# Kernel optimization log

Hardware: AMD Instinct MI355X
Metric: run time of the kernel (lower is better)

The kernel has to match this reference:

```python
import jax, jax.numpy as jnp
import numpy as np
from jax import lax

N_NODES = 100000
N_EDGES = 1600000
DIM = 64
N_GRAPHS = 128
OUT = 10
BN_EPS = 1e-5


def setup_inputs() -> dict:
    key = jax.random.key(0)
    ks = jax.random.split(key, 8)
    s = 1.0 / np.sqrt(DIM)
    x = jax.random.normal(ks[0], (N_NODES, DIM), dtype=jnp.float32)
    edge_index = jax.random.randint(ks[1], (2, N_EDGES), 0, N_NODES, dtype=jnp.int64)
    batch = jnp.sort(jax.random.randint(ks[2], (N_NODES,), 0, N_GRAPHS, dtype=jnp.int64))
    return {
        "x": x,
        "edge_index": edge_index,
        "batch": batch,
        "W1": jax.random.normal(ks[3], (5, DIM, DIM), dtype=jnp.float32) * s,
        "b1": jnp.zeros((5, DIM), jnp.float32),
        "gamma": jnp.ones((5, DIM), jnp.float32),
        "beta": jnp.zeros((5, DIM), jnp.float32),
        "rmean": jnp.zeros((5, DIM), jnp.float32),
        "rvar": jnp.ones((5, DIM), jnp.float32),
        "W2": jax.random.normal(ks[4], (5, DIM, DIM), dtype=jnp.float32) * s,
        "b2": jnp.zeros((5, DIM), jnp.float32),
        "lin1_w": jax.random.normal(ks[5], (DIM, DIM), dtype=jnp.float32) * s,
        "lin1_b": jnp.zeros((DIM,), jnp.float32),
        "lin2_w": jax.random.normal(ks[6], (DIM, OUT), dtype=jnp.float32) * s,
        "lin2_b": jnp.zeros((OUT,), jnp.float32),
    }


def reference(x, edge_index, batch, W1, b1, gamma, beta, rmean, rvar, W2, b2,
              lin1_w, lin1_b, lin2_w, lin2_b):
    n = x.shape[0]
    src, dst = edge_index[0], edge_index[1]

    def gin_layer(h, p):
        w1, bb1, g, bt, m, v, w2, bb2 = p
        # GINConv (eps=0): h_i <- MLP(h_i + sum_{j in N(i)} h_j)
        agg = jax.ops.segment_sum(h[src], dst, num_segments=n)
        h = h + agg
        h = h @ w1 + bb1
        h = (h - m) * lax.rsqrt(v + BN_EPS) * g + bt  # BatchNorm1d (eval)
        h = jax.nn.relu(h)
        h = jax.nn.relu(h @ w2 + bb2)
        return h, None

    h, _ = lax.scan(gin_layer, x, (W1, b1, gamma, beta, rmean, rvar, W2, b2))
    # global_add_pool over graphs in the batch
    pooled = jax.ops.segment_sum(h, batch, num_segments=N_GRAPHS)  # [G, dim]
    pooled = jax.nn.relu(pooled @ lin1_w + lin1_b)
    # dropout is identity in eval mode
    return pooled @ lin2_w + lin2_b  # [G, out]
```

## Files before the change

kernel.cpp:

```cpp
#include <hip/hip_runtime.h>

#define N_NODES  100000
#define N_EDGES  1600000
#define DIM      64
#define N_GRAPHS 128
#define OUT_DIM  10
#define SCAN_NB    196
#define SCAN_CHUNK 512
#define RANGE_BITS 14
#define RANGE_SIZE 16384
#define N_RANGES   7
#define NODE_PAD   (N_RANGES * RANGE_SIZE)
#define P_CHUNKS   512
#define P_EDGES    (N_EDGES / P_CHUNKS)
#define SUB        16

typedef unsigned int uint;
typedef unsigned short ushort;
typedef __attribute__((ext_vector_type(8))) short short8;
typedef __attribute__((ext_vector_type(4))) float f32x4;

__device__ __forceinline__ uint f2bf(float x) {
    uint b = __float_as_uint(x);
    b += 0x7fffu + ((b >> 16) & 1u);
    return b >> 16;
}


__global__ void count224_kernel(const int* __restrict__ dst, int* __restrict__ counts224) {
    __shared__ int cnt[8];
    const int c = blockIdx.x, tid = threadIdx.x;
    if (tid < 8) cnt[tid] = 0;
    __syncthreads();
    int c0 = 0, c1 = 0, c2 = 0, c3 = 0, c4 = 0, c5 = 0, c6 = 0;
    const int beg = c * P_EDGES, end = beg + P_EDGES;
    for (int i = beg + tid; i < end; i += 256) {
        int r = dst[i] >> RANGE_BITS;
        c0 += (r == 0); c1 += (r == 1); c2 += (r == 2); c3 += (r == 3);
        c4 += (r == 4); c5 += (r == 5); c6 += (r == 6);
    }
    atomicAdd(&cnt[0], c0); atomicAdd(&cnt[1], c1); atomicAdd(&cnt[2], c2);
    atomicAdd(&cnt[3], c3); atomicAdd(&cnt[4], c4); atomicAdd(&cnt[5], c5);
    atomicAdd(&cnt[6], c6);
    __syncthreads();
    if (tid < N_RANGES) counts224[tid * P_CHUNKS + c] = cnt[tid];
}

__global__ void scan224_kernel(const int* __restrict__ counts224, int* __restrict__ regionOff,
                               int* __restrict__ rangeStart) {
    __shared__ int sc[1024];
    const int t = threadIdx.x;
    const int NE = N_RANGES * P_CHUNKS;
    int v[4];
    int s = 0;
#pragma unroll
    for (int k = 0; k < 4; ++k) {
        const int idx = t * 4 + k;
        v[k] = (idx < NE) ? counts224[idx] : 0;
        s += v[k];
    }
    sc[t] = s;
    __syncthreads();
    for (int off = 1; off < 1024; off <<= 1) {
        int u = (t >= off) ? sc[t - off] : 0;
        __syncthreads();
        sc[t] += u;
        __syncthreads();
    }
    int base = sc[t] - s;
#pragma unroll
    for (int k = 0; k < 4; ++k) {
        const int idx = t * 4 + k;
        if (idx < NE) {
            regionOff[idx] = base;
            if ((idx & (P_CHUNKS - 1)) == 0) rangeStart[idx >> 9] = base;
            base += v[k];
        }
    }
    if (t == 1023) rangeStart[N_RANGES] = sc[1023];
}

__global__ __launch_bounds__(256) void partition_kernel(
    const int* __restrict__ src, const int* __restrict__ dst,
    const int* __restrict__ regionOff, uint2* __restrict__ epart) {
    __shared__ int pos[8];
    const int c = blockIdx.x, tid = threadIdx.x;
    if (tid < N_RANGES) pos[tid] = regionOff[tid * P_CHUNKS + c];
    __syncthreads();
    const int beg = c * P_EDGES, end = beg + P_EDGES;
    for (int i = beg + tid; i < end; i += 256) {
        int d = dst[i], s = src[i];
        int p = atomicAdd(&pos[d >> RANGE_BITS], 1);
        epart[p] = make_uint2((uint)s, (uint)d);
    }
}

__global__ __launch_bounds__(1024) void histoR_kernel(const uint2* __restrict__ epart,
                                                      const int* __restrict__ rangeStart,
                                                      int* __restrict__ countsS) {
    __shared__ int h[RANGE_SIZE];
    const int r = blockIdx.x & 7;
    if (r >= N_RANGES) return;
    const int s = blockIdx.x >> 3;
    const int tid = threadIdx.x;
    for (int j = tid; j < RANGE_SIZE; j += 1024) h[j] = 0;
    __syncthreads();
    const int e0 = rangeStart[r], e1 = rangeStart[r + 1];
    const int len = e1 - e0;
    const int a = e0 + (int)((long long)len * s / SUB);
    const int b = e0 + (int)((long long)len * (s + 1) / SUB);
    for (int i = a + tid; i < b; i += 1024)
        atomicAdd(&h[epart[i].y & (RANGE_SIZE - 1)], 1);
    __syncthreads();
    int* outp = countsS + (s * N_RANGES + r) * RANGE_SIZE;
    for (int j = tid; j < RANGE_SIZE; j += 1024) outp[j] = h[j];
}

__global__ void scanA_kernel(const int* __restrict__ countsS, int* __restrict__ blockSums, int n) {
    __shared__ int red[256];
    const int b = blockIdx.x, t = threadIdx.x;
    int sum = 0;
#pragma unroll
    for (int k = 0; k < 2; ++k) {
        const int node = b * SCAN_CHUNK + t * 2 + k;
        if (node < n) {
            const int r = node >> RANGE_BITS, jj = node & (RANGE_SIZE - 1);
            for (int s = 0; s < SUB; ++s)
                sum += countsS[(s * N_RANGES + r) * RANGE_SIZE + jj];
        }
    }
    red[t] = sum;
    __syncthreads();
    for (int off = 128; off > 0; off >>= 1) {
        if (t < off) red[t] += red[t + off];
        __syncthreads();
    }
    if (t == 0) blockSums[b] = red[0];
}

__global__ void scanB_kernel(const int* __restrict__ blockSums, int* __restrict__ blockOffs,
                             int* __restrict__ row_ptr) {
    __shared__ int sc[256];
    const int t = threadIdx.x;
    const int v = (t < SCAN_NB) ? blockSums[t] : 0;
    sc[t] = v;
    __syncthreads();
    for (int off = 1; off < 256; off <<= 1) {
        int u = (t >= off) ? sc[t - off] : 0;
        __syncthreads();
        sc[t] += u;
        __syncthreads();
    }
    if (t < SCAN_NB) blockOffs[t] = sc[t] - v;
    if (t == 255) row_ptr[N_NODES] = sc[255];
}

__global__ void scanC_kernel(const int* __restrict__ countsS, const int* __restrict__ blockOffs,
                             int* __restrict__ row_ptr, int* __restrict__ baseS, int n) {
    __shared__ int sc[256];
    const int b = blockIdx.x, t = threadIdx.x;
    const int node0 = b * SCAN_CHUNK + t * 2;
    int cnt0[SUB], cnt1[SUB];
    int tot0 = 0, tot1 = 0;
    if (node0 < n) {
        const int r = node0 >> RANGE_BITS, jj = node0 & (RANGE_SIZE - 1);
        for (int s = 0; s < SUB; ++s) {
            cnt0[s] = countsS[(s * N_RANGES + r) * RANGE_SIZE + jj];
            tot0 += cnt0[s];
        }
    }
    if (node0 + 1 < n) {
        const int r = (node0 + 1) >> RANGE_BITS, jj = (node0 + 1) & (RANGE_SIZE - 1);
        for (int s = 0; s < SUB; ++s) {
            cnt1[s] = countsS[(s * N_RANGES + r) * RANGE_SIZE + jj];
            tot1 += cnt1[s];
        }
    }
    const int ssum = tot0 + tot1;
    sc[t] = ssum;
    __syncthreads();
    for (int off = 1; off < 256; off <<= 1) {
        int u = (t >= off) ? sc[t - off] : 0;
        __syncthreads();
        sc[t] += u;
        __syncthreads();
    }
    const int pre = blockOffs[b] + sc[t] - ssum;
    if (node0 < n) {
        row_ptr[node0] = pre;
        int run = pre;
        for (int s = 0; s < SUB; ++s) { baseS[s * NODE_PAD + node0] = run; run += cnt0[s]; }
    }
    if (node0 + 1 < n) {
        const int pre1 = pre + tot0;
        row_ptr[node0 + 1] = pre1;
        int run = pre1;
        for (int s = 0; s < SUB; ++s) { baseS[s * NODE_PAD + node0 + 1] = run; run += cnt1[s]; }
    }
}

__global__ __launch_bounds__(1024) void fillR_kernel(const uint2* __restrict__ epart,
                                                     const int* __restrict__ rangeStart,
                                                     const int* __restrict__ baseS,
                                                     int* __restrict__ col_idx) {
    __shared__ int slots[RANGE_SIZE];
    const int r = blockIdx.x & 7;
    if (r >= N_RANGES) return;
    const int s = blockIdx.x >> 3;
    const int tid = threadIdx.x;
    const int* bp = baseS + s * NODE_PAD + r * RANGE_SIZE;
    for (int j = tid; j < RANGE_SIZE; j += 1024) slots[j] = bp[j];
    __syncthreads();
    const int e0 = rangeStart[r], e1 = rangeStart[r + 1];
    const int len = e1 - e0;
    const int a = e0 + (int)((long long)len * s / SUB);
    const int b = e0 + (int)((long long)len * (s + 1) / SUB);
    for (int i = a + tid; i < b; i += 1024) {
        uint2 e = epart[i];
        int pos = atomicAdd(&slots[e.y & (RANGE_SIZE - 1)], 1);
        col_idx[pos] = (int)e.x;
    }
}


__global__ void cvt_kernel(const float* __restrict__ x, ushort* __restrict__ xb, int n4) {
    int idx = blockIdx.x * blockDim.x + threadIdx.x;
    if (idx >= n4) return;
    float4 v = ((const float4*)x)[idx];
    uint2 o;
    o.x = f2bf(v.x) | (f2bf(v.y) << 16);
    o.y = f2bf(v.z) | (f2bf(v.w) << 16);
    ((uint2*)xb)[idx] = o;
}


__global__ void repack_kernel(const float* __restrict__ W1, const float* __restrict__ W2,
                              uint4* __restrict__ Wp) {
    const int wave = (blockIdx.x * blockDim.x + threadIdx.x) >> 6;
    if (wave >= 10) return;
    const int layer = wave >> 1;
    const float* W = (wave & 1) ? (W2 + layer * 4096) : (W1 + layer * 4096);
    const int lane = threadIdx.x & 63;
    const int n15 = lane & 15, quad = lane >> 4;
#pragma unroll
    for (int f = 0; f < 8; ++f) {
        const int outer = f >> 1, h = f & 1;
        uint p[4];
#pragma unroll
        for (int pj = 0; pj < 4; ++pj) {
            const int k0 = h * 32 + quad * 8 + 2 * pj;
            uint lo = f2bf(W[k0 * 64 + outer * 16 + n15]);
            uint hi = f2bf(W[(k0 + 1) * 64 + outer * 16 + n15]);
            p[pj] = lo | (hi << 16);
        }
        Wp[(wave * 8 + f) * 64 + lane] = make_uint4(p[0], p[1], p[2], p[3]);
    }
}


__device__ __forceinline__ void add_unpack(float acc[8], uint4 v) {
    acc[0] += __uint_as_float(v.x << 16);
    acc[1] += __uint_as_float(v.x & 0xffff0000u);
    acc[2] += __uint_as_float(v.y << 16);
    acc[3] += __uint_as_float(v.y & 0xffff0000u);
    acc[4] += __uint_as_float(v.z << 16);
    acc[5] += __uint_as_float(v.z & 0xffff0000u);
    acc[6] += __uint_as_float(v.w << 16);
    acc[7] += __uint_as_float(v.w & 0xffff0000u);
}

__global__ __launch_bounds__(256) void agg_kernel(
    const ushort* __restrict__ hb, ushort* __restrict__ tb,
    const int* __restrict__ row_ptr, const int* __restrict__ col_idx, int n)
{
    const uint4* __restrict__ hb4 = (const uint4*)hb;
    const int lane = threadIdx.x & 63;
    const int g = lane >> 3;
    const int q = lane & 7;
    const int wave = (blockIdx.x * blockDim.x + threadIdx.x) >> 6;
    const int i = wave * 8 + g;
    if (i >= n) return;
    const int rp0 = row_ptr[i];
    const int deg = row_ptr[i + 1] - rp0;

    float acc[8];
    {
        uint4 v = hb4[(size_t)i * 8 + q];
        acc[0] = __uint_as_float(v.x << 16);
        acc[1] = __uint_as_float(v.x & 0xffff0000u);
        acc[2] = __uint_as_float(v.y << 16);
        acc[3] = __uint_as_float(v.y & 0xffff0000u);
        acc[4] = __uint_as_float(v.z << 16);
        acc[5] = __uint_as_float(v.z & 0xffff0000u);
        acc[6] = __uint_as_float(v.w << 16);
        acc[7] = __uint_as_float(v.w & 0xffff0000u);
    }

    int e = 0;
    for (; e + 8 <= deg; e += 8) {
        int ix[8];
#pragma unroll
        for (int k = 0; k < 8; ++k) ix[k] = col_idx[rp0 + e + k];
        uint4 v[8];
#pragma unroll
        for (int k = 0; k < 8; ++k) v[k] = hb4[(size_t)ix[k] * 8 + q];
#pragma unroll
        for (int k = 0; k < 8; ++k) add_unpack(acc, v[k]);
    }
    if (e + 4 <= deg) {
        int ix[4];
#pragma unroll
        for (int k = 0; k < 4; ++k) ix[k] = col_idx[rp0 + e + k];
        uint4 v[4];
#pragma unroll
        for (int k = 0; k < 4; ++k) v[k] = hb4[(size_t)ix[k] * 8 + q];
#pragma unroll
        for (int k = 0; k < 4; ++k) add_unpack(acc, v[k]);
        e += 4;
    }
    for (; e < deg; ++e) {
        int ix = col_idx[rp0 + e];
        uint4 v = hb4[(size_t)ix * 8 + q];
        add_unpack(acc, v);
    }

    uint4 o;
    o.x = f2bf(acc[0]) | (f2bf(acc[1]) << 16);
    o.y = f2bf(acc[2]) | (f2bf(acc[3]) << 16);
    o.z = f2bf(acc[4]) | (f2bf(acc[5]) << 16);
    o.w = f2bf(acc[6]) | (f2bf(acc[7]) << 16);
    ((uint4*)tb)[(size_t)i * 8 + q] = o;
}


__global__ __launch_bounds__(256) void mlp_kernel(
    const ushort* __restrict__ tb, ushort* __restrict__ hb,
    const uint4* __restrict__ Wp,
    const float* __restrict__ b1, const float* __restrict__ gamma,
    const float* __restrict__ beta, const float* __restrict__ rmean,
    const float* __restrict__ rvar, const float* __restrict__ b2, int ntiles)
{
    __shared__ __align__(16) ushort U[4][16][72];
    const int lane = threadIdx.x & 63;
    const int wid  = threadIdx.x >> 6;
    const int n15  = lane & 15, quad = lane >> 4;

    short8 w1f[8], w2f[8];
    const short8* Wp8 = (const short8*)Wp;
#pragma unroll
    for (int f = 0; f < 8; ++f) {
        w1f[f] = Wp8[f * 64 + lane];
        w2f[f] = Wp8[(8 + f) * 64 + lane];
    }
    f32x4 sc[4], sh[4];
#pragma unroll
    for (int mt = 0; mt < 4; ++mt) {
        const int j0 = mt * 16 + quad * 4;
#pragma unroll
        for (int r = 0; r < 4; ++r) {
            float s = gamma[j0 + r] * rsqrtf(rvar[j0 + r] + 1e-5f);
            sc[mt][r] = s;
            sh[mt][r] = (b1[j0 + r] - rmean[j0 + r]) * s + beta[j0 + r];
        }
    }
    float bb2[4];
#pragma unroll
    for (int tc = 0; tc < 4; ++tc) bb2[tc] = b2[tc * 16 + n15];

    const int wave = blockIdx.x * 4 + wid;
    const int nwaves = gridDim.x * 4;
    for (int tile = wave; tile < ntiles; tile += nwaves) {
        const int nb = tile * 16;
        const short8* trow = (const short8*)(tb + (size_t)(nb + n15) * 64);
        short8 t0 = trow[quad];
        short8 t1 = trow[4 + quad];

        f32x4 c1[4];
#pragma unroll
        for (int mt = 0; mt < 4; ++mt) {
            c1[mt] = (f32x4){0.f, 0.f, 0.f, 0.f};
            c1[mt] = __builtin_amdgcn_mfma_f32_16x16x32_bf16(w1f[mt * 2 + 0], t0, c1[mt], 0, 0, 0);
            c1[mt] = __builtin_amdgcn_mfma_f32_16x16x32_bf16(w1f[mt * 2 + 1], t1, c1[mt], 0, 0, 0);
        }
#pragma unroll
        for (int mt = 0; mt < 4; ++mt) {
            float u0 = fmaxf(c1[mt][0] * sc[mt][0] + sh[mt][0], 0.f);
            float u1 = fmaxf(c1[mt][1] * sc[mt][1] + sh[mt][1], 0.f);
            float u2 = fmaxf(c1[mt][2] * sc[mt][2] + sh[mt][2], 0.f);
            float u3 = fmaxf(c1[mt][3] * sc[mt][3] + sh[mt][3], 0.f);
            uint2 pk;
            pk.x = f2bf(u0) | (f2bf(u1) << 16);
            pk.y = f2bf(u2) | (f2bf(u3) << 16);
            *(uint2*)&U[wid][n15][mt * 16 + quad * 4] = pk;
        }
        __threadfence_block();
        short8 u0 = *(const short8*)&U[wid][n15][quad * 8];
        short8 u1 = *(const short8*)&U[wid][n15][32 + quad * 8];

        f32x4 c2[4];
#pragma unroll
        for (int tc = 0; tc < 4; ++tc) {
            c2[tc] = (f32x4){0.f, 0.f, 0.f, 0.f};
            c2[tc] = __builtin_amdgcn_mfma_f32_16x16x32_bf16(u0, w2f[tc * 2 + 0], c2[tc], 0, 0, 0);
            c2[tc] = __builtin_amdgcn_mfma_f32_16x16x32_bf16(u1, w2f[tc * 2 + 1], c2[tc], 0, 0, 0);
        }
#pragma unroll
        for (int tc = 0; tc < 4; ++tc) {
#pragma unroll
            for (int r = 0; r < 4; ++r) {
                float v = fmaxf(c2[tc][r] + bb2[tc], 0.f);
                hb[(size_t)(nb + quad * 4 + r) * 64 + tc * 16 + n15] = (ushort)f2bf(v);
            }
        }
    }
}


__global__ void pool_kernel(const ushort* __restrict__ hb, const int* __restrict__ batch,
                            float* __restrict__ pooled, int n) {
    const int lane = threadIdx.x & 63;
    const int wid  = threadIdx.x >> 6;
    const int wave = blockIdx.x * 4 + wid;
    const int nwaves = gridDim.x * 4;
    const int per = (n + nwaves - 1) / nwaves;
    const int a = wave * per;
    const int b = min(a + per, n);
    if (a >= b) return;
    int cur = batch[a];
    float sum = 0.0f;
    for (int i = a; i < b; ++i) {
        int g = batch[i];
        if (g != cur) {
            atomicAdd(&pooled[cur * DIM + lane], sum);
            sum = 0.0f;
            cur = g;
        }
        sum += __uint_as_float(((uint)hb[(size_t)i * DIM + lane]) << 16);
    }
    atomicAdd(&pooled[cur * DIM + lane], sum);
}


__global__ void head_kernel(const float* __restrict__ pooled,
                            const float* __restrict__ w1, const float* __restrict__ b1,
                            const float* __restrict__ w2, const float* __restrict__ b2,
                            float* __restrict__ out) {
    const int g = blockIdx.x;
    const int lane = threadIdx.x;
    __shared__ float pl[DIM];
    __shared__ float y1l[DIM];
    pl[lane] = pooled[g * DIM + lane];
    __syncthreads();
    float y = b1[lane];
#pragma unroll
    for (int d = 0; d < DIM; ++d) y += pl[d] * w1[d * DIM + lane];
    y1l[lane] = fmaxf(y, 0.0f);
    __syncthreads();
    if (lane < OUT_DIM) {
        float y2 = b2[lane];
#pragma unroll
        for (int d = 0; d < DIM; ++d) y2 += y1l[d] * w2[d * OUT_DIM + lane];
        out[g * OUT_DIM + lane] = y2;
    }
}


extern "C" void kernel_launch(void* const* d_in, const int* in_sizes, int n_in,
                              void* d_out, int out_size, void* d_ws, size_t ws_size,
                              hipStream_t stream) {
    const float* x     = (const float*)d_in[0];
    const int*   eidx  = (const int*)  d_in[1];
    const int*   batch = (const int*)  d_in[2];
    const float* W1    = (const float*)d_in[3];
    const float* b1    = (const float*)d_in[4];
    const float* gamma = (const float*)d_in[5];
    const float* beta  = (const float*)d_in[6];
    const float* rmean = (const float*)d_in[7];
    const float* rvar  = (const float*)d_in[8];
    const float* W2    = (const float*)d_in[9];
    const float* b2    = (const float*)d_in[10];
    const float* l1w   = (const float*)d_in[11];
    const float* l1b   = (const float*)d_in[12];
    const float* l2w   = (const float*)d_in[13];
    const float* l2b   = (const float*)d_in[14];
    float* out = (float*)d_out;

    const size_t CS = (size_t)SUB * N_RANGES * RANGE_SIZE;
    const size_t BS = (size_t)SUB * NODE_PAD;
    const size_t NR = (size_t)N_RANGES * P_CHUNKS;
    int* counts224  = (int*)d_ws;
    int* regionOff  = counts224 + 3584;
    int* rangeStart = regionOff + 3584;
    int* blockSums  = rangeStart + 64;
    int* blockOffs  = blockSums + 256;
    int* row_ptr    = blockOffs + 256;
    int* countsS    = row_ptr + 100352;
    int* baseS      = countsS + CS;
    uint2* epart    = (uint2*)(baseS + BS);
    int* col_idx    = (int*)(epart + N_EDGES);
    uint4* Wp       = (uint4*)(col_idx + 1600000);
    ushort* tb      = (ushort*)(Wp + 5120);
    ushort* hb      = tb + (size_t)N_NODES * DIM;
    float* pooled   = (float*)(hb + (size_t)N_NODES * DIM);
    (void)NR;

    const int* srcp = eidx;
    const int* dstp = eidx + N_EDGES;

    hipMemsetAsync(pooled, 0, N_GRAPHS * DIM * sizeof(float), stream);

    cvt_kernel<<<(N_NODES * DIM / 4 + 255) / 256, 256, 0, stream>>>(x, hb, N_NODES * DIM / 4);
    repack_kernel<<<1, 640, 0, stream>>>(W1, W2, Wp);
    count224_kernel<<<P_CHUNKS, 256, 0, stream>>>(dstp, counts224);
    scan224_kernel<<<1, 1024, 0, stream>>>(counts224, regionOff, rangeStart);
    partition_kernel<<<P_CHUNKS, 256, 0, stream>>>(srcp, dstp, regionOff, epart);
    histoR_kernel<<<SUB * 8, 1024, 0, stream>>>(epart, rangeStart, countsS);
    scanA_kernel<<<SCAN_NB, 256, 0, stream>>>(countsS, blockSums, N_NODES);
    scanB_kernel<<<1, 256, 0, stream>>>(blockSums, blockOffs, row_ptr);
    scanC_kernel<<<SCAN_NB, 256, 0, stream>>>(countsS, blockOffs, row_ptr, baseS, N_NODES);
    fillR_kernel<<<SUB * 8, 1024, 0, stream>>>(epart, rangeStart, baseS, col_idx);

    const int agg_blocks = ((N_NODES + 7) / 8 * 64 + 255) / 256;
    const int ntiles = N_NODES / 16;

    for (int l = 0; l < 5; ++l) {
        agg_kernel<<<agg_blocks, 256, 0, stream>>>(hb, tb, row_ptr, col_idx, N_NODES);
        mlp_kernel<<<512, 256, 0, stream>>>(
            tb, hb, Wp + (size_t)l * 2 * 8 * 64,
            b1 + (size_t)l * DIM, gamma + (size_t)l * DIM, beta + (size_t)l * DIM,
            rmean + (size_t)l * DIM, rvar + (size_t)l * DIM, b2 + (size_t)l * DIM, ntiles);
    }
    pool_kernel<<<2048, 256, 0, stream>>>(hb, batch, pooled, N_NODES);
    head_kernel<<<N_GRAPHS, 64, 0, stream>>>(pooled, l1w, l1b, l2w, l2b, out);
}
```

Baseline: 413.7 us.

## Fuse neighbor aggregation into GIN MLP kernel with ping-pong feature buffers

Merges the separate CSR gather-sum kernel and the MFMA MLP kernel into one persistent kernel. Each wave aggregates its 16-node tile into shared memory and feeds it straight into the MLP, so the intermediate tb tensor is never written to or read from global memory and one launch per layer is dropped. Because other waves still read the previous layer's features, the layer output goes to a second buffer and the two buffers swap each layer. The risk is that the fused kernel runs only 512 blocks with higher register and LDS use, which lowers occupancy for the latency-bound random gathers compared with the standalone aggregation grid.

```diff
diff --git a/kernel.cpp b/kernel.cpp
--- a/kernel.cpp
+++ b/kernel.cpp
@@ -269,81 +269,22 @@
     acc[7] += __uint_as_float(v.w & 0xffff0000u);
 }
 
-__global__ __launch_bounds__(256) void agg_kernel(
-    const ushort* __restrict__ hb, ushort* __restrict__ tb,
-    const int* __restrict__ row_ptr, const int* __restrict__ col_idx, int n)
-{
-    const uint4* __restrict__ hb4 = (const uint4*)hb;
-    const int lane = threadIdx.x & 63;
-    const int g = lane >> 3;
-    const int q = lane & 7;
-    const int wave = (blockIdx.x * blockDim.x + threadIdx.x) >> 6;
-    const int i = wave * 8 + g;
-    if (i >= n) return;
-    const int rp0 = row_ptr[i];
-    const int deg = row_ptr[i + 1] - rp0;
-
-    float acc[8];
-    {
-        uint4 v = hb4[(size_t)i * 8 + q];
-        acc[0] = __uint_as_float(v.x << 16);
-        acc[1] = __uint_as_float(v.x & 0xffff0000u);
-        acc[2] = __uint_as_float(v.y << 16);
-        acc[3] = __uint_as_float(v.y & 0xffff0000u);
-        acc[4] = __uint_as_float(v.z << 16);
-        acc[5] = __uint_as_float(v.z & 0xffff0000u);
-        acc[6] = __uint_as_float(v.w << 16);
-        acc[7] = __uint_as_float(v.w & 0xffff0000u);
-    }
-
-    int e = 0;
-    for (; e + 8 <= deg; e += 8) {
-        int ix[8];
-#pragma unroll
-        for (int k = 0; k < 8; ++k) ix[k] = col_idx[rp0 + e + k];
-        uint4 v[8];
-#pragma unroll
-        for (int k = 0; k < 8; ++k) v[k] = hb4[(size_t)ix[k] * 8 + q];
-#pragma unroll
-        for (int k = 0; k < 8; ++k) add_unpack(acc, v[k]);
-    }
-    if (e + 4 <= deg) {
-        int ix[4];
-#pragma unroll
-        for (int k = 0; k < 4; ++k) ix[k] = col_idx[rp0 + e + k];
-        uint4 v[4];
-#pragma unroll
-        for (int k = 0; k < 4; ++k) v[k] = hb4[(size_t)ix[k] * 8 + q];
-#pragma unroll
-        for (int k = 0; k < 4; ++k) add_unpack(acc, v[k]);
-        e += 4;
-    }
-    for (; e < deg; ++e) {
-        int ix = col_idx[rp0 + e];
-        uint4 v = hb4[(size_t)ix * 8 + q];
-        add_unpack(acc, v);
-    }
-
-    uint4 o;
-    o.x = f2bf(acc[0]) | (f2bf(acc[1]) << 16);
-    o.y = f2bf(acc[2]) | (f2bf(acc[3]) << 16);
-    o.z = f2bf(acc[4]) | (f2bf(acc[5]) << 16);
-    o.w = f2bf(acc[6]) | (f2bf(acc[7]) << 16);
-    ((uint4*)tb)[(size_t)i * 8 + q] = o;
-}
-
-
-__global__ __launch_bounds__(256) void mlp_kernel(
-    const ushort* __restrict__ tb, ushort* __restrict__ hb,
+__global__ __launch_bounds__(256) void gin_fused_kernel(
+    const ushort* __restrict__ hin, ushort* __restrict__ hout,
+    const int* __restrict__ row_ptr, const int* __restrict__ col_idx,
     const uint4* __restrict__ Wp,
     const float* __restrict__ b1, const float* __restrict__ gamma,
     const float* __restrict__ beta, const float* __restrict__ rmean,
     const float* __restrict__ rvar, const float* __restrict__ b2, int ntiles)
 {
+    __shared__ __align__(16) ushort T[4][16][72];
     __shared__ __align__(16) ushort U[4][16][72];
+    const uint4* __restrict__ hb4 = (const uint4*)hin;
     const int lane = threadIdx.x & 63;
     const int wid  = threadIdx.x >> 6;
     const int n15  = lane & 15, quad = lane >> 4;
+    const int g = lane >> 3;
+    const int q = lane & 7;
 
     short8 w1f[8], w2f[8];
     const short8* Wp8 = (const short8*)Wp;
@@ -371,9 +312,60 @@
     const int nwaves = gridDim.x * 4;
     for (int tile = wave; tile < ntiles; tile += nwaves) {
         const int nb = tile * 16;
-        const short8* trow = (const short8*)(tb + (size_t)(nb + n15) * 64);
-        short8 t0 = trow[quad];
-        short8 t1 = trow[4 + quad];
+#pragma unroll
+        for (int p = 0; p < 2; ++p) {
+            const int i = nb + p * 8 + g;
+            const int rp0 = row_ptr[i];
+            const int deg = row_ptr[i + 1] - rp0;
+            float acc[8];
+            {
+                uint4 v = hb4[(size_t)i * 8 + q];
+                acc[0] = __uint_as_float(v.x << 16);
+                acc[1] = __uint_as_float(v.x & 0xffff0000u);
+                acc[2] = __uint_as_float(v.y << 16);
+                acc[3] = __uint_as_float(v.y & 0xffff0000u);
+                acc[4] = __uint_as_float(v.z << 16);
+                acc[5] = __uint_as_float(v.z & 0xffff0000u);
+                acc[6] = __uint_as_float(v.w << 16);
+                acc[7] = __uint_as_float(v.w & 0xffff0000u);
+            }
+            int e = 0;
+            for (; e + 8 <= deg; e += 8) {
+                int ix[8];
+#pragma unroll
+                for (int k = 0; k < 8; ++k) ix[k] = col_idx[rp0 + e + k];
+                uint4 v[8];
+#pragma unroll
+                for (int k = 0; k < 8; ++k) v[k] = hb4[(size_t)ix[k] * 8 + q];
+#pragma unroll
+                for (int k = 0; k < 8; ++k) add_unpack(acc, v[k]);
+            }
+            if (e + 4 <= deg) {
+                int ix[4];
+#pragma unroll
+                for (int k = 0; k < 4; ++k) ix[k] = col_idx[rp0 + e + k];
+                uint4 v[4];
+#pragma unroll
+                for (int k = 0; k < 4; ++k) v[k] = hb4[(size_t)ix[k] * 8 + q];
+#pragma unroll
+                for (int k = 0; k < 4; ++k) add_unpack(acc, v[k]);
+                e += 4;
+            }
+            for (; e < deg; ++e) {
+                int ix = col_idx[rp0 + e];
+                uint4 v = hb4[(size_t)ix * 8 + q];
+                add_unpack(acc, v);
+            }
+            uint4 o;
+            o.x = f2bf(acc[0]) | (f2bf(acc[1]) << 16);
+            o.y = f2bf(acc[2]) | (f2bf(acc[3]) << 16);
+            o.z = f2bf(acc[4]) | (f2bf(acc[5]) << 16);
+            o.w = f2bf(acc[6]) | (f2bf(acc[7]) << 16);
+            *(uint4*)&T[wid][p * 8 + g][q * 8] = o;
+        }
+        __threadfence_block();
+        short8 t0 = *(const short8*)&T[wid][n15][quad * 8];
+        short8 t1 = *(const short8*)&T[wid][n15][32 + quad * 8];
 
         f32x4 c1[4];
 #pragma unroll
@@ -409,7 +401,7 @@
 #pragma unroll
             for (int r = 0; r < 4; ++r) {
                 float v = fmaxf(c2[tc][r] + bb2[tc], 0.f);
-                hb[(size_t)(nb + quad * 4 + r) * 64 + tc * 16 + n15] = (ushort)f2bf(v);
+                hout[(size_t)(nb + quad * 4 + r) * 64 + tc * 16 + n15] = (ushort)f2bf(v);
             }
         }
     }
@@ -487,7 +479,6 @@
 
     const size_t CS = (size_t)SUB * N_RANGES * RANGE_SIZE;
     const size_t BS = (size_t)SUB * NODE_PAD;
-    const size_t NR = (size_t)N_RANGES * P_CHUNKS;
     int* counts224  = (int*)d_ws;
     int* regionOff  = counts224 + 3584;
     int* rangeStart = regionOff + 3584;
@@ -499,17 +490,16 @@
     uint2* epart    = (uint2*)(baseS + BS);
     int* col_idx    = (int*)(epart + N_EDGES);
     uint4* Wp       = (uint4*)(col_idx + 1600000);
-    ushort* tb      = (ushort*)(Wp + 5120);
-    ushort* hb      = tb + (size_t)N_NODES * DIM;
-    float* pooled   = (float*)(hb + (size_t)N_NODES * DIM);
-    (void)NR;
+    ushort* hbA     = (ushort*)(Wp + 5120);
+    ushort* hbB     = hbA + (size_t)N_NODES * DIM;
+    float* pooled   = (float*)(hbB + (size_t)N_NODES * DIM);
 
     const int* srcp = eidx;
     const int* dstp = eidx + N_EDGES;
 
     hipMemsetAsync(pooled, 0, N_GRAPHS * DIM * sizeof(float), stream);
 
-    cvt_kernel<<<(N_NODES * DIM / 4 + 255) / 256, 256, 0, stream>>>(x, hb, N_NODES * DIM / 4);
+    cvt_kernel<<<(N_NODES * DIM / 4 + 255) / 256, 256, 0, stream>>>(x, hbA, N_NODES * DIM / 4);
     repack_kernel<<<1, 640, 0, stream>>>(W1, W2, Wp);
     count224_kernel<<<P_CHUNKS, 256, 0, stream>>>(dstp, counts224);
     scan224_kernel<<<1, 1024, 0, stream>>>(counts224, regionOff, rangeStart);
@@ -520,16 +510,16 @@
     scanC_kernel<<<SCAN_NB, 256, 0, stream>>>(countsS, blockOffs, row_ptr, baseS, N_NODES);
     fillR_kernel<<<SUB * 8, 1024, 0, stream>>>(epart, rangeStart, baseS, col_idx);
 
-    const int agg_blocks = ((N_NODES + 7) / 8 * 64 + 255) / 256;
     const int ntiles = N_NODES / 16;
-
+    ushort* hin  = hbA;
+    ushort* hout = hbB;
     for (int l = 0; l < 5; ++l) {
-        agg_kernel<<<agg_blocks, 256, 0, stream>>>(hb, tb, row_ptr, col_idx, N_NODES);
-        mlp_kernel<<<512, 256, 0, stream>>>(
-            tb, hb, Wp + (size_t)l * 2 * 8 * 64,
+        gin_fused_kernel<<<512, 256, 0, stream>>>(
+            hin, hout, row_ptr, col_idx, Wp + (size_t)l * 2 * 8 * 64,
             b1 + (size_t)l * DIM, gamma + (size_t)l * DIM, beta + (size_t)l * DIM,
             rmean + (size_t)l * DIM, rvar + (size_t)l * DIM, b2 + (size_t)l * DIM, ntiles);
-    }
-    pool_kernel<<<2048, 256, 0, stream>>>(hb, batch, pooled, N_NODES);
+        ushort* tmp = hin; hin = hout; hout = tmp;
+    }
+    pool_kernel<<<2048, 256, 0, stream>>>(hin, batch, pooled, N_NODES);
     head_kernel<<<N_GRAPHS, 64, 0, stream>>>(pooled, l1w, l1b, l2w, l2b, out);
 }
```

New measurement: 434.6 us. +5.1%, slower.
